# Optimization experiments

Hardware: AMD Instinct MI355X
Metric: run time of the kernel (lower is better)

The kernel has to match this reference:

```python
import jax, jax.numpy as jnp
import numpy as np

D_Z, D_A = 128, 64
D = D_Z + D_A            # 192
H1, H2 = 512, 512
E, S = 16, 1
B, N = 64, 2048
LN_EPS = 1e-5


def mish(x):
    return x * jnp.tanh(jax.nn.softplus(x))


def layernorm(x, g, b):
    m = jnp.mean(x, axis=-1, keepdims=True)
    v = jnp.mean((x - m) ** 2, axis=-1, keepdims=True)
    return (x - m) * jax.lax.rsqrt(v + LN_EPS) * g + b


def setup_inputs() -> dict:
    key = jax.random.key(0)
    ks = jax.random.split(key, 12)
    inp = {
        "z": jax.random.normal(ks[0], (B, N, D_Z), jnp.float32),
        "a": jax.random.normal(ks[1], (B, N, D_A), jnp.float32),
        "phi": jax.random.normal(ks[2], (D, E, S), jnp.float32) / np.sqrt(D),
        # stacked per-expert params (vectorized over e)
        "W1": jax.random.normal(ks[3], (E, D, H1), jnp.float32) / np.sqrt(D),
        "b1": jnp.zeros((E, H1), jnp.float32),
        "g1": jnp.ones((E, H1), jnp.float32),
        "be1": jnp.zeros((E, H1), jnp.float32),
        "W2": jax.random.normal(ks[4], (E, H1, H2), jnp.float32) / np.sqrt(H1),
        "b2": jnp.zeros((E, H2), jnp.float32),
        "g2": jnp.ones((E, H2), jnp.float32),
        "be2": jnp.zeros((E, H2), jnp.float32),
        "W3": jax.random.normal(ks[5], (E, H2, D_Z), jnp.float32) / np.sqrt(H2),
        "b3": jnp.zeros((E, D_Z), jnp.float32),
    }
    return inp


def reference(z, a, phi, W1, b1, g1, be1, W2, b2, g2, be2, W3, b3):
    x = jnp.concatenate([z, a], axis=-1)                      # [B,N,D]
    weights = jnp.einsum('bnd,des->bnes', x, phi)             # [B,N,E,S]
    dispatch = jax.nn.softmax(weights, axis=1)                # over tokens N
    xin = jnp.einsum('bnes,bnd->besd', dispatch, x)           # [B,E,S,D]
    # batched per-expert MLP: NormedLinear -> NormedLinear -> Linear
    h = jnp.einsum('besd,edh->besh', xin, W1) + b1[None, :, None, :]
    h = mish(layernorm(h, g1[None, :, None, :], be1[None, :, None, :]))
    h = jnp.einsum('besh,ehk->besk', h, W2) + b2[None, :, None, :]
    h = mish(layernorm(h, g2[None, :, None, :], be2[None, :, None, :]))
    out_e = jnp.einsum('besk,ekz->besz', h, W3) + b3[None, :, None, :]
    expert_outputs = out_e.reshape(out_e.shape[0], E * S, D_Z)    # b (e s) z
    combine = jax.nn.softmax(weights.reshape(weights.shape[0], weights.shape[1], E * S), axis=-1)
    out = jnp.einsum('bnk,bkz->bnz', combine, expert_outputs)     # [B,N,d_z]
    return out
```

## Files before the change

### kernel.cpp

```cpp
#include <hip/hip_runtime.h>
#include <math.h>

#define BB 64
#define NN 2048
#define DZ 128
#define DA 64
#define DD 192
#define EE 16
#define HH 512
#define LN_EPS 1e-5f

typedef __attribute__((ext_vector_type(8))) short short8;
typedef __attribute__((ext_vector_type(4))) float f32x4;

__device__ __forceinline__ float mishf(float x) {
    float sp = (x > 20.f) ? x : log1pf(__expf(x));
    return x * tanhf(sp);
}

__device__ __forceinline__ unsigned short bf16_rne(float f) {
    unsigned u = __float_as_uint(f);
    return (unsigned short)((u + 0x7FFFu + ((u >> 16) & 1u)) >> 16);
}
__device__ __forceinline__ float bf16f(unsigned short h) {
    return __uint_as_float(((unsigned)h) << 16);
}

__global__ __launch_bounds__(256)
void k_phipack(const float* __restrict__ phi, unsigned short* __restrict__ ph,
               unsigned short* __restrict__ pl) {
    int idx = blockIdx.x * 256 + threadIdx.x;
    if (idx >= 6 * 64 * 8) return;
    int j = idx & 7, lane = (idx >> 3) & 63, kk = idx >> 9;
    int e = lane & 15, g = lane >> 4;
    int d = kk * 32 + g * 8 + j;
    float f = phi[d * EE + e];
    unsigned short h = bf16_rne(f);
    ph[idx] = h;
    pl[idx] = bf16_rne(f - bf16f(h));
}

__global__ __launch_bounds__(256)
void k_weights(const float* __restrict__ z, const float* __restrict__ a,
               const unsigned short* __restrict__ php,
               const unsigned short* __restrict__ plp,
               float* __restrict__ w) {
    int t = threadIdx.x;
    int wv = t >> 6, l = t & 63;
    long tokbase = ((long)blockIdx.x * 4 + wv) * 16;
    long tokA = tokbase + (l & 15);
    int g = l >> 4;

    short8 bh[6], bl[6], ah[6], al[6];
#pragma unroll
    for (int kk = 0; kk < 6; kk++) {
        bh[kk] = *(const short8*)(php + kk * 512 + l * 8);
        bl[kk] = *(const short8*)(plp + kk * 512 + l * 8);
    }
#pragma unroll
    for (int kk = 0; kk < 6; kk++) {
        int d0 = kk * 32 + g * 8;
        const float* src = (d0 < DZ) ? (z + tokA * DZ + d0)
                                     : (a + tokA * DA + (d0 - DZ));
        float4 v0 = ((const float4*)src)[0];
        float4 v1 = ((const float4*)src)[1];
        float f[8] = {v0.x, v0.y, v0.z, v0.w, v1.x, v1.y, v1.z, v1.w};
#pragma unroll
        for (int j = 0; j < 8; j++) {
            unsigned short h = bf16_rne(f[j]);
            ah[kk][j] = (short)h;
            al[kk][j] = (short)bf16_rne(f[j] - bf16f(h));
        }
    }

    f32x4 acc = {0.f, 0.f, 0.f, 0.f};
#pragma unroll
    for (int kk = 0; kk < 6; kk++)
        acc = __builtin_amdgcn_mfma_f32_16x16x32_bf16(ah[kk], bh[kk], acc, 0, 0, 0);
#pragma unroll
    for (int kk = 0; kk < 6; kk++)
        acc = __builtin_amdgcn_mfma_f32_16x16x32_bf16(al[kk], bh[kk], acc, 0, 0, 0);
#pragma unroll
    for (int kk = 0; kk < 6; kk++)
        acc = __builtin_amdgcn_mfma_f32_16x16x32_bf16(ah[kk], bl[kk], acc, 0, 0, 0);

    int e = l & 15;
#pragma unroll
    for (int r = 0; r < 4; r++) {
        long row = tokbase + g * 4 + r;
        w[row * EE + e] = acc[r];
    }
}

#define RSTR 17
__global__ __launch_bounds__(256)
void k_stats1(const float* __restrict__ w, float* __restrict__ lmax,
              float* __restrict__ lsum) {
    __shared__ float red[256 * RSTR];
    int b = blockIdx.y, c = blockIdx.x, t = threadIdx.x;
    const float* wb = w + ((long)b * NN + c * 512) * EE;

    float m[EE];
#pragma unroll
    for (int e = 0; e < EE; e++) m[e] = -1e30f;
    for (int k = 0; k < 2; k++) {
        const float4* row = (const float4*)(wb + ((long)(k * 256 + t)) * EE);
#pragma unroll
        for (int q = 0; q < 4; q++) {
            float4 v = row[q];
            m[q * 4 + 0] = fmaxf(m[q * 4 + 0], v.x);
            m[q * 4 + 1] = fmaxf(m[q * 4 + 1], v.y);
            m[q * 4 + 2] = fmaxf(m[q * 4 + 2], v.z);
            m[q * 4 + 3] = fmaxf(m[q * 4 + 3], v.w);
        }
    }
#pragma unroll
    for (int e = 0; e < EE; e++) red[t * RSTR + e] = m[e];
    __syncthreads();
    for (int s = 128; s > 0; s >>= 1) {
        if (t < s) {
#pragma unroll
            for (int e = 0; e < EE; e++)
                red[t * RSTR + e] = fmaxf(red[t * RSTR + e], red[(t + s) * RSTR + e]);
        }
        __syncthreads();
    }
    float mg[EE];
#pragma unroll
    for (int e = 0; e < EE; e++) mg[e] = red[e];
    __syncthreads();

    float s_[EE];
#pragma unroll
    for (int e = 0; e < EE; e++) s_[e] = 0.f;
    for (int k = 0; k < 2; k++) {
        const float4* row = (const float4*)(wb + ((long)(k * 256 + t)) * EE);
#pragma unroll
        for (int q = 0; q < 4; q++) {
            float4 v = row[q];
            s_[q * 4 + 0] += __expf(v.x - mg[q * 4 + 0]);
            s_[q * 4 + 1] += __expf(v.y - mg[q * 4 + 1]);
            s_[q * 4 + 2] += __expf(v.z - mg[q * 4 + 2]);
            s_[q * 4 + 3] += __expf(v.w - mg[q * 4 + 3]);
        }
    }
#pragma unroll
    for (int e = 0; e < EE; e++) red[t * RSTR + e] = s_[e];
    __syncthreads();
    for (int s = 128; s > 0; s >>= 1) {
        if (t < s) {
#pragma unroll
            for (int e = 0; e < EE; e++)
                red[t * RSTR + e] += red[(t + s) * RSTR + e];
        }
        __syncthreads();
    }
    if (t < EE) {
        lmax[((long)b * 4 + c) * EE + t] = mg[t];
        lsum[((long)b * 4 + c) * EE + t] = red[t];
    }
}

__global__ __launch_bounds__(256)
void k_stats2(const float* __restrict__ lmax, const float* __restrict__ lsum,
              float* __restrict__ gmax, float* __restrict__ grcp) {
    int idx = blockIdx.x * 256 + threadIdx.x;
    if (idx >= BB * EE) return;
    int b = idx >> 4, e = idx & 15;
    float gm = -1e30f;
#pragma unroll
    for (int c = 0; c < 4; c++)
        gm = fmaxf(gm, lmax[((long)b * 4 + c) * EE + e]);
    float Z = 0.f;
#pragma unroll
    for (int c = 0; c < 4; c++)
        Z += __expf(lmax[((long)b * 4 + c) * EE + e] - gm) * lsum[((long)b * 4 + c) * EE + e];
    gmax[idx] = gm;
    grcp[idx] = 1.f / Z;
}

__global__ __launch_bounds__(256)
void k_xin2(const float* __restrict__ z, const float* __restrict__ a,
            const float* __restrict__ w, const float* __restrict__ gmax,
            const float* __restrict__ grcp, float* __restrict__ pxin) {
    int kq = blockIdx.x, b = blockIdx.y;
    int t = threadIdx.x, wv = t >> 6, l = t & 63;
    int g = l >> 4, c = l & 15;

    float gm = gmax[b * EE + c];
    float gr = grcp[b * EE + c];
    const float* wb = w + ((long)b * NN + (long)kq * 128) * EE;
    const float* zb = z + ((long)b * NN + (long)kq * 128) * DZ;
    const float* ab = a + ((long)b * NN + (long)kq * 128) * DA;

    f32x4 acc0 = {0.f, 0.f, 0.f, 0.f};
    f32x4 acc1 = {0.f, 0.f, 0.f, 0.f};
    f32x4 acc2 = {0.f, 0.f, 0.f, 0.f};

#pragma unroll
    for (int kk = 0; kk < 4; kk++) {
        int nb = kk * 32 + g * 8;
        short8 ad;
#pragma unroll
        for (int j = 0; j < 8; j++) {
            float wvv = wb[(long)(nb + j) * EE + c];
            ad[j] = (short)bf16_rne(__expf(wvv - gm) * gr);
        }
#pragma unroll
        for (int i = 0; i < 3; i++) {
            int d = (wv * 3 + i) * 16 + c;
            short8 xh_, xl_;
#pragma unroll
            for (int j = 0; j < 8; j++) {
                float f = (d < DZ) ? zb[(long)(nb + j) * DZ + d]
                                   : ab[(long)(nb + j) * DA + (d - DZ)];
                unsigned short h = bf16_rne(f);
                xh_[j] = (short)h;
                xl_[j] = (short)bf16_rne(f - bf16f(h));
            }
            if (i == 0) {
                acc0 = __builtin_amdgcn_mfma_f32_16x16x32_bf16(ad, xh_, acc0, 0, 0, 0);
                acc0 = __builtin_amdgcn_mfma_f32_16x16x32_bf16(ad, xl_, acc0, 0, 0, 0);
            } else if (i == 1) {
                acc1 = __builtin_amdgcn_mfma_f32_16x16x32_bf16(ad, xh_, acc1, 0, 0, 0);
                acc1 = __builtin_amdgcn_mfma_f32_16x16x32_bf16(ad, xl_, acc1, 0, 0, 0);
            } else {
                acc2 = __builtin_amdgcn_mfma_f32_16x16x32_bf16(ad, xh_, acc2, 0, 0, 0);
                acc2 = __builtin_amdgcn_mfma_f32_16x16x32_bf16(ad, xl_, acc2, 0, 0, 0);
            }
        }
    }

    float* pb = pxin + (long)kq * (EE * BB * DD) + (long)b * DD;
#pragma unroll
    for (int r = 0; r < 4; r++) {
        int e = g * 4 + r;
        float* pr = pb + (long)e * (BB * DD);
        pr[(wv * 3 + 0) * 16 + c] = acc0[r];
        pr[(wv * 3 + 1) * 16 + c] = acc1[r];
        pr[(wv * 3 + 2) * 16 + c] = acc2[r];
    }
}

__global__ __launch_bounds__(192)
void k_xin_scalar(const float* __restrict__ z, const float* __restrict__ a,
                  const float* __restrict__ w, const float* __restrict__ gmax,
                  const float* __restrict__ grcp, float* __restrict__ dst) {
    __shared__ float disp[128 * EE];
    int b = blockIdx.y, chunk = blockIdx.x, t = threadIdx.x;

    const float* wrow = w + ((long)b * NN + (long)chunk * 128) * EE;
    for (int i = t; i < 128 * EE; i += 192) {
        int e = i & 15;
        disp[i] = __expf(wrow[i] - gmax[b * EE + e]) * grcp[b * EE + e];
    }
    __syncthreads();

    const float* xp;
    int stride;
    if (t < DZ) { xp = z + ((long)b * NN + (long)chunk * 128) * DZ + t; stride = DZ; }
    else        { xp = a + ((long)b * NN + (long)chunk * 128) * DA + (t - DZ); stride = DA; }

    float acc[EE];
#pragma unroll
    for (int e = 0; e < EE; e++) acc[e] = 0.f;

    for (int n = 0; n < 128; n++) {
        float xv = xp[(long)n * stride];
        const float4* dp = (const float4*)(disp + n * EE);
#pragma unroll
        for (int q = 0; q < 4; q++) {
            float4 p = dp[q];
            acc[q * 4 + 0] += p.x * xv;
            acc[q * 4 + 1] += p.y * xv;
            acc[q * 4 + 2] += p.z * xv;
            acc[q * 4 + 3] += p.w * xv;
        }
    }
#pragma unroll
    for (int e = 0; e < EE; e++)
        atomicAdd(&dst[((long)e * BB + b) * DD + t], acc[e]);
}

__global__ __launch_bounds__(256)
void k_xinred(const float* __restrict__ xinp, float* __restrict__ xin) {
    long i = (long)blockIdx.x * 256 + threadIdx.x;
    float s = 0.f;
#pragma unroll
    for (int c = 0; c < 16; c++)
        s += xinp[(long)c * (EE * BB * DD) + i];
    xin[i] = s;
}

template<int K, int OUT, int KSLICE, bool ADD_BIAS>
__global__ __launch_bounds__(256)
void k_gemm(const float* __restrict__ X, const float* __restrict__ W,
            const float* __restrict__ bias, float* __restrict__ Yp) {
    constexpr int SP = KSLICE + 4;
    constexpr int K4 = KSLICE / 4;
    __shared__ float xs[64 * SP];

    int cb = blockIdx.x, ks = blockIdx.y, e = blockIdx.z;
    int t = threadIdx.x;
    int k0 = ks * KSLICE;

    for (int i = t; i < 64 * K4; i += 256) {
        int r = i / K4, k4 = i % K4;
        *(float4*)&xs[r * SP + k4 * 4] =
            *(const float4*)(X + ((long)e * BB + r) * K + k0 + k4 * 4);
    }
    __syncthreads();

    int c = cb * 32 + (t & 7) * 4;
    int r0 = (t >> 3) * 2;
    const float* Wp = W + ((long)e * K + k0) * OUT + c;

    float acc0[4], acc1[4];
#pragma unroll
    for (int j = 0; j < 4; j++) {
        float bv = ADD_BIAS ? bias[(long)e * OUT + c + j] : 0.f;
        acc0[j] = bv;
        acc1[j] = bv;
    }

#pragma unroll 4
    for (int k4 = 0; k4 < K4; k4++) {
        float4 x0 = *(const float4*)&xs[r0 * SP + k4 * 4];
        float4 x1 = *(const float4*)&xs[(r0 + 1) * SP + k4 * 4];
        const float* xp0 = &x0.x;
        const float* xp1 = &x1.x;
#pragma unroll
        for (int j = 0; j < 4; j++) {
            float4 wv = *(const float4*)(Wp + (long)(k4 * 4 + j) * OUT);
            float xa = xp0[j], xb = xp1[j];
            acc0[0] += xa * wv.x; acc0[1] += xa * wv.y;
            acc0[2] += xa * wv.z; acc0[3] += xa * wv.w;
            acc1[0] += xb * wv.x; acc1[1] += xb * wv.y;
            acc1[2] += xb * wv.z; acc1[3] += xb * wv.w;
        }
    }

    float* yp = Yp + ((long)ks * (EE * BB) + (long)e * BB + r0) * OUT + c;
    *(float4*)yp         = make_float4(acc0[0], acc0[1], acc0[2], acc0[3]);
    *(float4*)(yp + OUT) = make_float4(acc1[0], acc1[1], acc1[2], acc1[3]);
}

template<int KS, bool HAS_BIAS>
__global__ __launch_bounds__(256)
void k_lnact(const float* __restrict__ Yp, const float* __restrict__ bias,
             const float* __restrict__ g, const float* __restrict__ be,
             float* __restrict__ Yo) {
    __shared__ float redS[4], redQ[4];
    int row = blockIdx.x, t = threadIdx.x;
    int e = row >> 6;

    float v[2];
#pragma unroll
    for (int j = 0; j < 2; j++) {
        int cj = t + j * 256;
        float s = HAS_BIAS ? bias[(long)e * HH + cj] : 0.f;
#pragma unroll
        for (int ks = 0; ks < KS; ks++)
            s += Yp[((long)ks * (EE * BB) + row) * HH + cj];
        v[j] = s;
    }
    float s = v[0] + v[1];
    float q = v[0] * v[0] + v[1] * v[1];
    for (int off = 32; off > 0; off >>= 1) {
        s += __shfl_xor(s, off);
        q += __shfl_xor(q, off);
    }
    int wave = t >> 6, lane = t & 63;
    if (lane == 0) { redS[wave] = s; redQ[wave] = q; }
    __syncthreads();
    float S = redS[0] + redS[1] + redS[2] + redS[3];
    float Q = redQ[0] + redQ[1] + redQ[2] + redQ[3];
    float mean = S * (1.f / HH);
    float var = Q * (1.f / HH) - mean * mean;
    float rstd = rsqrtf(var + LN_EPS);

#pragma unroll
    for (int j = 0; j < 2; j++) {
        int cj = t + j * 256;
        float gg = g[(long)e * HH + cj], bb = be[(long)e * HH + cj];
        Yo[(long)row * HH + cj] = mishf((v[j] - mean) * rstd * gg + bb);
    }
}

template<int KS>
__global__ __launch_bounds__(256)
void k_fin3(const float* __restrict__ p3, const float* __restrict__ b3,
            float* __restrict__ eout) {
    int t = threadIdx.x;
    int row = blockIdx.x * 2 + (t >> 7);
    int c = t & 127;
    int e = row >> 6, b = row & 63;
    float s = b3[(long)e * DZ + c];
#pragma unroll
    for (int ks = 0; ks < KS; ks++)
        s += p3[((long)ks * (EE * BB) + row) * DZ + c];
    eout[((long)b * EE + e) * DZ + c] = s;
}

__global__ __launch_bounds__(256)
void k_combine(const float* __restrict__ w, const float* __restrict__ eout,
               float* __restrict__ out) {
    __shared__ float comb[64][EE];
    __shared__ float eo[EE * DZ];
    int b = blockIdx.y, n0 = blockIdx.x * 64, t = threadIdx.x;

    for (int i = t; i < EE * DZ; i += 256) eo[i] = eout[(long)b * EE * DZ + i];

    int tok = t >> 2, sub = t & 3;
    const float4 wv = *(const float4*)(w + ((long)b * NN + n0 + tok) * EE + sub * 4);
    float mx = fmaxf(fmaxf(wv.x, wv.y), fmaxf(wv.z, wv.w));
    mx = fmaxf(mx, __shfl_xor(mx, 1, 4));
    mx = fmaxf(mx, __shfl_xor(mx, 2, 4));
    float e0 = __expf(wv.x - mx), e1 = __expf(wv.y - mx);
    float e2 = __expf(wv.z - mx), e3 = __expf(wv.w - mx);
    float s = e0 + e1 + e2 + e3;
    s += __shfl_xor(s, 1, 4);
    s += __shfl_xor(s, 2, 4);
    float rs = 1.f / s;
    comb[tok][sub * 4 + 0] = e0 * rs;
    comb[tok][sub * 4 + 1] = e1 * rs;
    comb[tok][sub * 4 + 2] = e2 * rs;
    comb[tok][sub * 4 + 3] = e3 * rs;
    __syncthreads();

    for (int i = t; i < 64 * DZ; i += 256) {
        int tk = i >> 7, c = i & 127;
        float acc = 0.f;
#pragma unroll
        for (int e = 0; e < EE; e++) acc += comb[tk][e] * eo[e * DZ + c];
        out[((long)b * NN + n0 + tk) * DZ + c] = acc;
    }
}

extern "C" void kernel_launch(void* const* d_in, const int* in_sizes, int n_in,
                              void* d_out, int out_size, void* d_ws, size_t ws_size,
                              hipStream_t stream) {
    const float* z   = (const float*)d_in[0];
    const float* a   = (const float*)d_in[1];
    const float* phi = (const float*)d_in[2];
    const float* W1  = (const float*)d_in[3];
    const float* b1  = (const float*)d_in[4];
    const float* g1  = (const float*)d_in[5];
    const float* be1 = (const float*)d_in[6];
    const float* W2  = (const float*)d_in[7];
    const float* b2  = (const float*)d_in[8];
    const float* g2  = (const float*)d_in[9];
    const float* be2 = (const float*)d_in[10];
    const float* W3  = (const float*)d_in[11];
    const float* b3  = (const float*)d_in[12];
    float* out = (float*)d_out;

    char* p = (char*)d_ws;
    float* w    = (float*)p; p += (size_t)BB * NN * EE * 4;
    float* gmax = (float*)p; p += (size_t)BB * EE * 4;
    float* grcp = (float*)p; p += (size_t)BB * EE * 4;
    float* lmax = (float*)p; p += (size_t)BB * 4 * EE * 4;
    float* lsum = (float*)p; p += (size_t)BB * 4 * EE * 4;
    float* xin  = (float*)p; p += (size_t)BB * EE * DD * 4;
    unsigned short* php = (unsigned short*)p; p += 6 * 64 * 8 * 2;
    unsigned short* plp = (unsigned short*)p; p += 6 * 64 * 8 * 2;
    char* region = p;
    float* pxin = (float*)region;
    float* part = (float*)region;
    float* h1   = (float*)(region + (size_t)4 * EE * BB * HH * 4);
    float* h2   = h1;
    float* eout = (float*)(region + (size_t)4 * EE * BB * HH * 4
                                  + (size_t)EE * BB * HH * 4);
    size_t region_off = (size_t)(region - (char*)d_ws);
    size_t need_full = region_off + (size_t)16 * EE * BB * DD * 4;
    bool full = ws_size >= need_full;

    k_phipack<<<12, 256, 0, stream>>>(phi, php, plp);
    k_weights<<<BB * NN / 64, 256, 0, stream>>>(z, a, php, plp, w);
    k_stats1<<<dim3(4, BB), 256, 0, stream>>>(w, lmax, lsum);
    k_stats2<<<4, 256, 0, stream>>>(lmax, lsum, gmax, grcp);

    if (full) {
        k_xin2<<<dim3(16, BB), 256, 0, stream>>>(z, a, w, gmax, grcp, pxin);
        k_xinred<<<EE * BB * DD / 256, 256, 0, stream>>>(pxin, xin);
    } else {
        hipMemsetAsync(xin, 0, (size_t)BB * EE * DD * 4, stream);
        k_xin_scalar<<<dim3(NN / 128, BB), 192, 0, stream>>>(z, a, w, gmax, grcp, xin);
    }

    k_gemm<DD, HH, 96, false>
        <<<dim3(HH / 32, 2, EE), 256, 0, stream>>>(xin, W1, nullptr, part);
    k_lnact<2, true><<<EE * BB, 256, 0, stream>>>(part, b1, g1, be1, h1);

    k_gemm<HH, HH, 128, false>
        <<<dim3(HH / 32, 4, EE), 256, 0, stream>>>(h1, W2, nullptr, part);
    k_lnact<4, true><<<EE * BB, 256, 0, stream>>>(part, b2, g2, be2, h2);

    k_gemm<HH, DZ, 64, false>
        <<<dim3(DZ / 32, 8, EE), 256, 0, stream>>>(h2, W3, nullptr, part);
    k_fin3<8><<<EE * BB / 2, 256, 0, stream>>>(part, b3, eout);

    k_combine<<<dim3(NN / 64, BB), 256, 0, stream>>>(w, eout, out);
}
```

Before: 134.4 us.

## Double-buffer xin2 token tiles in LDS via direct global-to-LDS loads

The dispatch-weighted reduction kernel now stages each 32-token chunk of z, a and the routing logits into shared memory with global_load_lds, double-buffered so the next chunk loads while the current one feeds the MFMAs. Before this, each thread did strided scalar global reads. The change is meant to coalesce global traffic and hide load latency. It adds LDS usage (about 56 KB) and two barriers per iteration, and there is no explicit wait on the async LDS loads beyond __syncthreads.

```diff
diff --git a/kernel.cpp b/kernel.cpp
--- a/kernel.cpp
+++ b/kernel.cpp
@@ -24,6 +24,12 @@
 }
 __device__ __forceinline__ float bf16f(unsigned short h) {
     return __uint_as_float(((unsigned)h) << 16);
+}
+
+__device__ __forceinline__ void gload_lds16(const float* g, float* l) {
+    __builtin_amdgcn_global_load_lds(
+        (const __attribute__((address_space(1))) void*)g,
+        (__attribute__((address_space(3))) void*)l, 16, 0, 0);
 }
 
 __global__ __launch_bounds__(256)
@@ -183,27 +189,49 @@
 void k_xin2(const float* __restrict__ z, const float* __restrict__ a,
             const float* __restrict__ w, const float* __restrict__ gmax,
             const float* __restrict__ grcp, float* __restrict__ pxin) {
+    __shared__ float zs[2][32 * 128];
+    __shared__ float as_[2][32 * 64];
+    __shared__ float ws_[2][32 * 16];
     int kq = blockIdx.x, b = blockIdx.y;
     int t = threadIdx.x, wv = t >> 6, l = t & 63;
     int g = l >> 4, c = l & 15;
 
     float gm = gmax[b * EE + c];
     float gr = grcp[b * EE + c];
-    const float* wb = w + ((long)b * NN + (long)kq * 128) * EE;
     const float* zb = z + ((long)b * NN + (long)kq * 128) * DZ;
     const float* ab = a + ((long)b * NN + (long)kq * 128) * DA;
+    const float* wb = w + ((long)b * NN + (long)kq * 128) * EE;
+
+    auto stage = [&](int kk, int bf) {
+#pragma unroll
+        for (int s = 0; s < 4; s++) {
+            int seg = wv * 4 + s;
+            gload_lds16(zb + kk * 4096 + seg * 256 + l * 4, &zs[bf][seg * 256]);
+        }
+#pragma unroll
+        for (int s = 0; s < 2; s++) {
+            int seg = wv * 2 + s;
+            gload_lds16(ab + kk * 2048 + seg * 256 + l * 4, &as_[bf][seg * 256]);
+        }
+        if (wv < 2)
+            gload_lds16(wb + kk * 512 + wv * 256 + l * 4, &ws_[bf][wv * 256]);
+    };
 
     f32x4 acc0 = {0.f, 0.f, 0.f, 0.f};
     f32x4 acc1 = {0.f, 0.f, 0.f, 0.f};
     f32x4 acc2 = {0.f, 0.f, 0.f, 0.f};
 
+    stage(0, 0);
 #pragma unroll
     for (int kk = 0; kk < 4; kk++) {
-        int nb = kk * 32 + g * 8;
+        int bf = kk & 1;
+        if (kk < 3) stage(kk + 1, bf ^ 1);
+        __syncthreads();
+
         short8 ad;
 #pragma unroll
         for (int j = 0; j < 8; j++) {
-            float wvv = wb[(long)(nb + j) * EE + c];
+            float wvv = ws_[bf][(g * 8 + j) * 16 + c];
             ad[j] = (short)bf16_rne(__expf(wvv - gm) * gr);
         }
 #pragma unroll
@@ -212,8 +240,9 @@
             short8 xh_, xl_;
 #pragma unroll
             for (int j = 0; j < 8; j++) {
-                float f = (d < DZ) ? zb[(long)(nb + j) * DZ + d]
-                                   : ab[(long)(nb + j) * DA + (d - DZ)];
+                int n = g * 8 + j;
+                float f = (d < DZ) ? zs[bf][n * 128 + d]
+                                   : as_[bf][n * 64 + (d - DZ)];
                 unsigned short h = bf16_rne(f);
                 xh_[j] = (short)h;
                 xl_[j] = (short)bf16_rne(f - bf16f(h));
@@ -229,6 +258,7 @@
                 acc2 = __builtin_amdgcn_mfma_f32_16x16x32_bf16(ad, xl_, acc2, 0, 0, 0);
             }
         }
+        __syncthreads();
     }
 
     float* pb = pxin + (long)kq * (EE * BB * DD) + (long)b * DD;
```

Result: no change. 134.6 us (+0.2%).

## Fuse gating logits and dispatch accumulation into one pass over tokens

Applied to the files above, without the earlier changes.

A new kernel, k_wxin, reads each 32-token chunk of z and a once and stages them in shared memory as split bf16 hi/lo pairs. From that one copy it computes the gating logits with MFMA and, in the same block, accumulates exp(logit) times x into per-chunk partial sums. It also writes per-chunk partial softmax denominators, which a small reduction kernel combines before the dispatch result is scaled. This removes the second read of z/a and the separate max/sum statistics kernels. In exchange it drops the max subtraction in the token softmax, so very large logits could overflow, and it writes four times as many partial buffers (64 chunks instead of 16), which also raises the workspace needed for this path.

```diff
diff --git a/kernel.cpp b/kernel.cpp
--- a/kernel.cpp
+++ b/kernel.cpp
@@ -9,6 +9,7 @@
 #define EE 16
 #define HH 512
 #define LN_EPS 1e-5f
+#define NCH 64
 
 typedef __attribute__((ext_vector_type(8))) short short8;
 typedef __attribute__((ext_vector_type(4))) float f32x4;
@@ -41,6 +42,143 @@
 }
 
 __global__ __launch_bounds__(256)
+void k_wxin(const float* __restrict__ z, const float* __restrict__ a,
+            const unsigned short* __restrict__ php,
+            const unsigned short* __restrict__ plp,
+            float* __restrict__ w, float* __restrict__ pxin,
+            float* __restrict__ pZ) {
+    __shared__ unsigned int xhl[4 * 32 * 49];
+    __shared__ float wexp[32 * 17];
+    int ch = blockIdx.x, b = blockIdx.y;
+    int t = threadIdx.x, wv = t >> 6, l = t & 63;
+    int g = l >> 4, c = l & 15;
+    long tok0 = (long)b * NN + (long)ch * 32;
+
+    {
+        const float4* zp = (const float4*)(z + tok0 * DZ);
+        const float4* ap = (const float4*)(a + tok0 * DA);
+#pragma unroll
+        for (int k = 0; k < 6; k++) {
+            int f = t + k * 256;
+            int tok = f / 48, q = f - tok * 48;
+            float4 v = (q < 32) ? zp[tok * 32 + q] : ap[tok * 16 + (q - 32)];
+            int reg = q / 12;
+            int dq = q * 4 - reg * 48;
+            unsigned* dst = &xhl[(reg * 32 + tok) * 49 + dq];
+            const float* pv = &v.x;
+#pragma unroll
+            for (int i = 0; i < 4; i++) {
+                unsigned short h = bf16_rne(pv[i]);
+                unsigned short lo = bf16_rne(pv[i] - bf16f(h));
+                dst[i] = ((unsigned)h << 16) | (unsigned)lo;
+            }
+        }
+    }
+    __syncthreads();
+
+    short8 xh0, xl0, xh1, xl1, xh2, xl2;
+#pragma unroll
+    for (int j = 0; j < 8; j++) {
+        int rowb = (wv * 32 + g * 8 + j) * 49;
+        unsigned u0 = xhl[rowb + c];
+        unsigned u1 = xhl[rowb + 16 + c];
+        unsigned u2 = xhl[rowb + 32 + c];
+        xh0[j] = (short)(u0 >> 16); xl0[j] = (short)(u0 & 0xffff);
+        xh1[j] = (short)(u1 >> 16); xl1[j] = (short)(u1 & 0xffff);
+        xh2[j] = (short)(u2 >> 16); xl2[j] = (short)(u2 & 0xffff);
+    }
+
+    if (wv < 2) {
+        f32x4 accw = {0.f, 0.f, 0.f, 0.f};
+#pragma unroll
+        for (int kk = 0; kk < 6; kk++) {
+            short8 bh = *(const short8*)(php + kk * 512 + l * 8);
+            short8 bl = *(const short8*)(plp + kk * 512 + l * 8);
+            int dbase = kk * 32 + g * 8;
+            int reg = dbase / 48;
+            int dq = dbase - reg * 48;
+            int rowb = (reg * 32 + wv * 16 + c) * 49 + dq;
+            short8 ah, al;
+#pragma unroll
+            for (int j = 0; j < 8; j++) {
+                unsigned u = xhl[rowb + j];
+                ah[j] = (short)(u >> 16);
+                al[j] = (short)(u & 0xffff);
+            }
+            accw = __builtin_amdgcn_mfma_f32_16x16x32_bf16(ah, bh, accw, 0, 0, 0);
+            accw = __builtin_amdgcn_mfma_f32_16x16x32_bf16(al, bh, accw, 0, 0, 0);
+            accw = __builtin_amdgcn_mfma_f32_16x16x32_bf16(ah, bl, accw, 0, 0, 0);
+        }
+#pragma unroll
+        for (int r = 0; r < 4; r++) {
+            long row_g = tok0 + wv * 16 + g * 4 + r;
+            w[row_g * EE + c] = accw[r];
+            wexp[(wv * 16 + g * 4 + r) * 17 + c] = __expf(accw[r]);
+        }
+    }
+    __syncthreads();
+
+    short8 ad;
+    float zl = 0.f;
+#pragma unroll
+    for (int j = 0; j < 8; j++) {
+        float wf = wexp[(g * 8 + j) * 17 + c];
+        ad[j] = (short)bf16_rne(wf);
+        zl += wf;
+    }
+    f32x4 acc0 = {0.f, 0.f, 0.f, 0.f};
+    f32x4 acc1 = {0.f, 0.f, 0.f, 0.f};
+    f32x4 acc2 = {0.f, 0.f, 0.f, 0.f};
+    acc0 = __builtin_amdgcn_mfma_f32_16x16x32_bf16(ad, xh0, acc0, 0, 0, 0);
+    acc0 = __builtin_amdgcn_mfma_f32_16x16x32_bf16(ad, xl0, acc0, 0, 0, 0);
+    acc1 = __builtin_amdgcn_mfma_f32_16x16x32_bf16(ad, xh1, acc1, 0, 0, 0);
+    acc1 = __builtin_amdgcn_mfma_f32_16x16x32_bf16(ad, xl1, acc1, 0, 0, 0);
+    acc2 = __builtin_amdgcn_mfma_f32_16x16x32_bf16(ad, xh2, acc2, 0, 0, 0);
+    acc2 = __builtin_amdgcn_mfma_f32_16x16x32_bf16(ad, xl2, acc2, 0, 0, 0);
+
+    if (wv == 0) {
+        zl += __shfl_xor(zl, 16);
+        zl += __shfl_xor(zl, 32);
+        if (l < 16) pZ[((long)ch * BB + b) * EE + c] = zl;
+    }
+
+    float* pb = pxin + (long)ch * (EE * BB * DD) + (long)b * DD;
+#pragma unroll
+    for (int r = 0; r < 4; r++) {
+        int e = g * 4 + r;
+        float* pr = pb + (long)e * (BB * DD);
+        pr[(wv * 3 + 0) * 16 + c] = acc0[r];
+        pr[(wv * 3 + 1) * 16 + c] = acc1[r];
+        pr[(wv * 3 + 2) * 16 + c] = acc2[r];
+    }
+}
+
+__global__ __launch_bounds__(256)
+void k_zred(const float* __restrict__ pZ, float* __restrict__ Zg) {
+    int idx = blockIdx.x * 256 + threadIdx.x;
+    if (idx >= BB * EE) return;
+    float s = 0.f;
+#pragma unroll 8
+    for (int ch = 0; ch < NCH; ch++)
+        s += pZ[(long)ch * (BB * EE) + idx];
+    Zg[idx] = 1.f / s;
+}
+
+__global__ __launch_bounds__(256)
+void k_xinred(const float* __restrict__ pxin, const float* __restrict__ Zg,
+              float* __restrict__ xin) {
+    long i = (long)blockIdx.x * 256 + threadIdx.x;
+    int e = (int)(i / (BB * DD));
+    int rem = (int)(i - (long)e * (BB * DD));
+    int b = rem / DD;
+    float s = 0.f;
+#pragma unroll 8
+    for (int ch = 0; ch < NCH; ch++)
+        s += pxin[(long)ch * (EE * BB * DD) + i];
+    xin[i] = s * Zg[b * EE + e];
+}
+
+__global__ __launch_bounds__(256)
 void k_weights(const float* __restrict__ z, const float* __restrict__ a,
                const unsigned short* __restrict__ php,
                const unsigned short* __restrict__ plp,
@@ -72,7 +210,6 @@
             al[kk][j] = (short)bf16_rne(f[j] - bf16f(h));
         }
     }
-
     f32x4 acc = {0.f, 0.f, 0.f, 0.f};
 #pragma unroll
     for (int kk = 0; kk < 6; kk++)
@@ -83,7 +220,6 @@
 #pragma unroll
     for (int kk = 0; kk < 6; kk++)
         acc = __builtin_amdgcn_mfma_f32_16x16x32_bf16(ah[kk], bl[kk], acc, 0, 0, 0);
-
     int e = l & 15;
 #pragma unroll
     for (int r = 0; r < 4; r++) {
@@ -99,7 +235,6 @@
     __shared__ float red[256 * RSTR];
     int b = blockIdx.y, c = blockIdx.x, t = threadIdx.x;
     const float* wb = w + ((long)b * NN + c * 512) * EE;
-
     float m[EE];
 #pragma unroll
     for (int e = 0; e < EE; e++) m[e] = -1e30f;
@@ -129,7 +264,6 @@
 #pragma unroll
     for (int e = 0; e < EE; e++) mg[e] = red[e];
     __syncthreads();
-
     float s_[EE];
 #pragma unroll
     for (int e = 0; e < EE; e++) s_[e] = 0.f;
@@ -179,92 +313,25 @@
     grcp[idx] = 1.f / Z;
 }
 
-__global__ __launch_bounds__(256)
-void k_xin2(const float* __restrict__ z, const float* __restrict__ a,
-            const float* __restrict__ w, const float* __restrict__ gmax,
-            const float* __restrict__ grcp, float* __restrict__ pxin) {
-    int kq = blockIdx.x, b = blockIdx.y;
-    int t = threadIdx.x, wv = t >> 6, l = t & 63;
-    int g = l >> 4, c = l & 15;
-
-    float gm = gmax[b * EE + c];
-    float gr = grcp[b * EE + c];
-    const float* wb = w + ((long)b * NN + (long)kq * 128) * EE;
-    const float* zb = z + ((long)b * NN + (long)kq * 128) * DZ;
-    const float* ab = a + ((long)b * NN + (long)kq * 128) * DA;
-
-    f32x4 acc0 = {0.f, 0.f, 0.f, 0.f};
-    f32x4 acc1 = {0.f, 0.f, 0.f, 0.f};
-    f32x4 acc2 = {0.f, 0.f, 0.f, 0.f};
-
-#pragma unroll
-    for (int kk = 0; kk < 4; kk++) {
-        int nb = kk * 32 + g * 8;
-        short8 ad;
-#pragma unroll
-        for (int j = 0; j < 8; j++) {
-            float wvv = wb[(long)(nb + j) * EE + c];
-            ad[j] = (short)bf16_rne(__expf(wvv - gm) * gr);
-        }
-#pragma unroll
-        for (int i = 0; i < 3; i++) {
-            int d = (wv * 3 + i) * 16 + c;
-            short8 xh_, xl_;
-#pragma unroll
-            for (int j = 0; j < 8; j++) {
-                float f = (d < DZ) ? zb[(long)(nb + j) * DZ + d]
-                                   : ab[(long)(nb + j) * DA + (d - DZ)];
-                unsigned short h = bf16_rne(f);
-                xh_[j] = (short)h;
-                xl_[j] = (short)bf16_rne(f - bf16f(h));
-            }
-            if (i == 0) {
-                acc0 = __builtin_amdgcn_mfma_f32_16x16x32_bf16(ad, xh_, acc0, 0, 0, 0);
-                acc0 = __builtin_amdgcn_mfma_f32_16x16x32_bf16(ad, xl_, acc0, 0, 0, 0);
-            } else if (i == 1) {
-                acc1 = __builtin_amdgcn_mfma_f32_16x16x32_bf16(ad, xh_, acc1, 0, 0, 0);
-                acc1 = __builtin_amdgcn_mfma_f32_16x16x32_bf16(ad, xl_, acc1, 0, 0, 0);
-            } else {
-                acc2 = __builtin_amdgcn_mfma_f32_16x16x32_bf16(ad, xh_, acc2, 0, 0, 0);
-                acc2 = __builtin_amdgcn_mfma_f32_16x16x32_bf16(ad, xl_, acc2, 0, 0, 0);
-            }
-        }
-    }
-
-    float* pb = pxin + (long)kq * (EE * BB * DD) + (long)b * DD;
-#pragma unroll
-    for (int r = 0; r < 4; r++) {
-        int e = g * 4 + r;
-        float* pr = pb + (long)e * (BB * DD);
-        pr[(wv * 3 + 0) * 16 + c] = acc0[r];
-        pr[(wv * 3 + 1) * 16 + c] = acc1[r];
-        pr[(wv * 3 + 2) * 16 + c] = acc2[r];
-    }
-}
-
 __global__ __launch_bounds__(192)
 void k_xin_scalar(const float* __restrict__ z, const float* __restrict__ a,
                   const float* __restrict__ w, const float* __restrict__ gmax,
                   const float* __restrict__ grcp, float* __restrict__ dst) {
     __shared__ float disp[128 * EE];
     int b = blockIdx.y, chunk = blockIdx.x, t = threadIdx.x;
-
     const float* wrow = w + ((long)b * NN + (long)chunk * 128) * EE;
     for (int i = t; i < 128 * EE; i += 192) {
         int e = i & 15;
         disp[i] = __expf(wrow[i] - gmax[b * EE + e]) * grcp[b * EE + e];
     }
     __syncthreads();
-
     const float* xp;
     int stride;
     if (t < DZ) { xp = z + ((long)b * NN + (long)chunk * 128) * DZ + t; stride = DZ; }
     else        { xp = a + ((long)b * NN + (long)chunk * 128) * DA + (t - DZ); stride = DA; }
-
     float acc[EE];
 #pragma unroll
     for (int e = 0; e < EE; e++) acc[e] = 0.f;
-
     for (int n = 0; n < 128; n++) {
         float xv = xp[(long)n * stride];
         const float4* dp = (const float4*)(disp + n * EE);
@@ -282,16 +349,6 @@
         atomicAdd(&dst[((long)e * BB + b) * DD + t], acc[e]);
 }
 
-__global__ __launch_bounds__(256)
-void k_xinred(const float* __restrict__ xinp, float* __restrict__ xin) {
-    long i = (long)blockIdx.x * 256 + threadIdx.x;
-    float s = 0.f;
-#pragma unroll
-    for (int c = 0; c < 16; c++)
-        s += xinp[(long)c * (EE * BB * DD) + i];
-    xin[i] = s;
-}
-
 template<int K, int OUT, int KSLICE, bool ADD_BIAS>
 __global__ __launch_bounds__(256)
 void k_gemm(const float* __restrict__ X, const float* __restrict__ W,
@@ -299,22 +356,18 @@
     constexpr int SP = KSLICE + 4;
     constexpr int K4 = KSLICE / 4;
     __shared__ float xs[64 * SP];
-
     int cb = blockIdx.x, ks = blockIdx.y, e = blockIdx.z;
     int t = threadIdx.x;
     int k0 = ks * KSLICE;
-
     for (int i = t; i < 64 * K4; i += 256) {
         int r = i / K4, k4 = i % K4;
         *(float4*)&xs[r * SP + k4 * 4] =
             *(const float4*)(X + ((long)e * BB + r) * K + k0 + k4 * 4);
     }
     __syncthreads();
-
     int c = cb * 32 + (t & 7) * 4;
     int r0 = (t >> 3) * 2;
     const float* Wp = W + ((long)e * K + k0) * OUT + c;
-
     float acc0[4], acc1[4];
 #pragma unroll
     for (int j = 0; j < 4; j++) {
@@ -322,7 +375,6 @@
         acc0[j] = bv;
         acc1[j] = bv;
     }
-
 #pragma unroll 4
     for (int k4 = 0; k4 < K4; k4++) {
         float4 x0 = *(const float4*)&xs[r0 * SP + k4 * 4];
@@ -339,7 +391,6 @@
             acc1[2] += xb * wv.z; acc1[3] += xb * wv.w;
         }
     }
-
     float* yp = Yp + ((long)ks * (EE * BB) + (long)e * BB + r0) * OUT + c;
     *(float4*)yp         = make_float4(acc0[0], acc0[1], acc0[2], acc0[3]);
     *(float4*)(yp + OUT) = make_float4(acc1[0], acc1[1], acc1[2], acc1[3]);
@@ -353,7 +404,6 @@
     __shared__ float redS[4], redQ[4];
     int row = blockIdx.x, t = threadIdx.x;
     int e = row >> 6;
-
     float v[2];
 #pragma unroll
     for (int j = 0; j < 2; j++) {
@@ -378,7 +428,6 @@
     float mean = S * (1.f / HH);
     float var = Q * (1.f / HH) - mean * mean;
     float rstd = rsqrtf(var + LN_EPS);
-
 #pragma unroll
     for (int j = 0; j < 2; j++) {
         int cj = t + j * 256;
@@ -408,9 +457,7 @@
     __shared__ float comb[64][EE];
     __shared__ float eo[EE * DZ];
     int b = blockIdx.y, n0 = blockIdx.x * 64, t = threadIdx.x;
-
     for (int i = t; i < EE * DZ; i += 256) eo[i] = eout[(long)b * EE * DZ + i];
-
     int tok = t >> 2, sub = t & 3;
     const float4 wv = *(const float4*)(w + ((long)b * NN + n0 + tok) * EE + sub * 4);
     float mx = fmaxf(fmaxf(wv.x, wv.y), fmaxf(wv.z, wv.w));
@@ -427,7 +474,6 @@
     comb[tok][sub * 4 + 2] = e2 * rs;
     comb[tok][sub * 4 + 3] = e3 * rs;
     __syncthreads();
-
     for (int i = t; i < 64 * DZ; i += 256) {
         int tk = i >> 7, c = i & 127;
         float acc = 0.f;
@@ -464,6 +510,8 @@
     float* xin  = (float*)p; p += (size_t)BB * EE * DD * 4;
     unsigned short* php = (unsigned short*)p; p += 6 * 64 * 8 * 2;
     unsigned short* plp = (unsigned short*)p; p += 6 * 64 * 8 * 2;
+    float* pZ   = (float*)p; p += (size_t)NCH * BB * EE * 4;
+    float* Zg   = (float*)p; p += (size_t)BB * EE * 4;
     char* region = p;
     float* pxin = (float*)region;
     float* part = (float*)region;
@@ -472,18 +520,19 @@
     float* eout = (float*)(region + (size_t)4 * EE * BB * HH * 4
                                   + (size_t)EE * BB * HH * 4);
     size_t region_off = (size_t)(region - (char*)d_ws);
-    size_t need_full = region_off + (size_t)16 * EE * BB * DD * 4;
+    size_t need_full = region_off + (size_t)NCH * EE * BB * DD * 4;
     bool full = ws_size >= need_full;
 
     k_phipack<<<12, 256, 0, stream>>>(phi, php, plp);
-    k_weights<<<BB * NN / 64, 256, 0, stream>>>(z, a, php, plp, w);
-    k_stats1<<<dim3(4, BB), 256, 0, stream>>>(w, lmax, lsum);
-    k_stats2<<<4, 256, 0, stream>>>(lmax, lsum, gmax, grcp);
 
     if (full) {
-        k_xin2<<<dim3(16, BB), 256, 0, stream>>>(z, a, w, gmax, grcp, pxin);
-        k_xinred<<<EE * BB * DD / 256, 256, 0, stream>>>(pxin, xin);
+        k_wxin<<<dim3(NCH, BB), 256, 0, stream>>>(z, a, php, plp, w, pxin, pZ);
+        k_zred<<<4, 256, 0, stream>>>(pZ, Zg);
+        k_xinred<<<EE * BB * DD / 256, 256, 0, stream>>>(pxin, Zg, xin);
     } else {
+        k_weights<<<BB * NN / 64, 256, 0, stream>>>(z, a, php, plp, w);
+        k_stats1<<<dim3(4, BB), 256, 0, stream>>>(w, lmax, lsum);
+        k_stats2<<<4, 256, 0, stream>>>(lmax, lsum, gmax, grcp);
         hipMemsetAsync(xin, 0, (size_t)BB * EE * DD * 4, stream);
         k_xin_scalar<<<dim3(NN / 128, BB), 192, 0, stream>>>(z, a, w, gmax, grcp, xin);
     }
```

New measurement: 127.6 us. 5.1% less time.
